# Kernel tuning notes

Hardware: AMD Instinct MI355X
Metric: run time of the kernel (lower is better)

The kernel has to match this reference:

```python
import jax, jax.numpy as jnp
import numpy as np

B, T, DIM = 1, 2048, 1024
NUM_HEADS, HEAD_DIM = 8, 128
ATTN_SCALE = 0.12


def _rms_norm(x):
    # F.rms_norm(x, x.size(-1)) with no weight; eps defaults to machine eps
    eps = jnp.asarray(jnp.finfo(x.dtype).eps, x.dtype)
    return x * jax.lax.rsqrt(jnp.mean(x * x, axis=-1, keepdims=True) + eps)


def _rotary_tables(seq_len, head_dim):
    # (1/1024) ** linspace(0,1,head_dim//4), then pad with head_dim//4 zeros
    freq = (1.0 / 1024.0) ** jnp.linspace(0.0, 1.0, head_dim // 4, dtype=jnp.float32)
    ang = jnp.concatenate([freq, jnp.zeros(head_dim // 4, jnp.float32)])  # [hd/2]
    theta = jnp.arange(seq_len, dtype=jnp.float32)[:, None] * ang[None, :]  # [T, hd/2]
    return jnp.cos(theta), jnp.sin(theta)


def _apply_rotary(x, cos, sin):
    # x: [B, T, H, hd]
    x1, x2 = jnp.split(x.astype(jnp.float32), 2, axis=-1)
    c = cos[None, :, None, :]
    s = sin[None, :, None, :]
    y1 = x1 * c + x2 * s
    y2 = -x1 * s + x2 * c
    return jnp.concatenate([y1, y2], axis=-1).astype(x.dtype)


def setup_inputs() -> dict:
    key = jax.random.key(0)
    ks = jax.random.split(key, 5)
    bound = (3.0 ** 0.5) * 0.5 * DIM ** (-0.5)
    x = jax.random.normal(ks[0], (B, T, DIM), jnp.float32)
    ve = jax.random.normal(ks[1], (B, T, NUM_HEADS * HEAD_DIM), jnp.float32)
    qkv_w = jax.random.uniform(ks[2], (3, NUM_HEADS * HEAD_DIM, DIM), jnp.float32, -bound, bound)
    lambdas = jnp.array([0.5, 0.5], jnp.float32)
    # original zero-inits c_proj; use small random weight so the output is nontrivial
    c_proj_w = jax.random.uniform(ks[3], (DIM, NUM_HEADS * HEAD_DIM), jnp.float32, -bound, bound)
    return {"x": x, "ve": ve, "qkv_w": qkv_w, "lambdas": lambdas, "c_proj_w": c_proj_w}


def reference(x, ve, qkv_w, lambdas, c_proj_w):
    Bx, Tx, D = x.shape
    H, hd = NUM_HEADS, HEAD_DIM
    # fused QKV projection: weight [3*H*hd, D]
    qkv = x @ qkv_w.reshape(3 * H * hd, D).T            # [B, T, 3*H*hd]
    qkv = qkv.reshape(Bx, Tx, 3 * H, hd)
    q, k, v = jnp.split(qkv, 3, axis=-2)                # each [B, T, H, hd]
    q, k = _rms_norm(q), _rms_norm(k)
    cos, sin = _rotary_tables(Tx, hd)
    q, k = _apply_rotary(q, cos, sin), _apply_rotary(k, cos, sin)
    v = lambdas[0] * v + lambdas[1] * ve.reshape(v.shape)
    att = jnp.einsum('bthd,bshd->bhts', q, k) * ATTN_SCALE
    causal = jnp.tril(jnp.ones((Tx, Tx), bool))
    att = jnp.where(causal[None, None], att, -jnp.inf)
    att = jax.nn.softmax(att, axis=-1)
    y = jnp.einsum('bhts,bshd->bthd', att, v).reshape(Bx, Tx, H * hd)
    return y @ c_proj_w.T
```

## Files before the change

### kernel.cpp

```cpp
#include <hip/hip_runtime.h>


typedef __attribute__((ext_vector_type(8))) short short8;
typedef __attribute__((ext_vector_type(4))) short short4b;
typedef __attribute__((ext_vector_type(4))) float fx4;
typedef __attribute__((ext_vector_type(8))) unsigned short ushort8;
typedef __attribute__((ext_vector_type(4))) unsigned short ushort4v;
typedef __attribute__((ext_vector_type(2))) unsigned short ushort2v;
typedef __attribute__((ext_vector_type(4))) float float4v;

#define T_SEQ 2048
#define NH 8
#define HD 128

__device__ __forceinline__ unsigned short f2bf(float f) {
  union { float f; unsigned u; } v; v.f = f;
  unsigned u = v.u;
  u += 0x7fffu + ((u >> 16) & 1u);
  return (unsigned short)(u >> 16);
}
__device__ __forceinline__ short bf_t(float f) {
  union { float f; unsigned u; } v; v.f = f;
  return (short)(v.u >> 16);
}
__device__ __forceinline__ float bf2f(unsigned short h) {
  union { unsigned u; float f; } v; v.u = ((unsigned)h) << 16;
  return v.f;
}

typedef __attribute__((address_space(1))) unsigned int glb_u32;
typedef __attribute__((address_space(3))) unsigned int lds_u32;
__device__ __forceinline__ void gl_lds16(const unsigned short* g, unsigned short* l) {
  __builtin_amdgcn_global_load_lds((const glb_u32*)g, (lds_u32*)l, 16, 0, 0);
}

__global__ __launch_bounds__(256) void cast3_kernel(
    const float* __restrict__ x, const float* __restrict__ w1,
    const float* __restrict__ w2, unsigned short* __restrict__ o) {
  long q = (long)blockIdx.x * 256 + threadIdx.x;
  const float* src;
  if (q < 524288)        src = x  + 4 * q;
  else if (q < 1310720)  src = w1 + 4 * (q - 524288);
  else                   src = w2 + 4 * (q - 1310720);
  float4v v = *(const float4v*)src;
  ushort4v r;
  r[0] = f2bf(v[0]); r[1] = f2bf(v[1]); r[2] = f2bf(v[2]); r[3] = f2bf(v[3]);
  *(ushort4v*)(o + 4 * q) = r;
}

template <bool OUT_BF16, int BM, int BN, int MINW>
__global__ __launch_bounds__(256, MINW) void gemm_bt4(
    const unsigned short* __restrict__ A, const unsigned short* __restrict__ B,
    void* __restrict__ Cp, int M, int N, int K) {
  constexpr int MT = BM / 32;
  constexpr int NT = BN / 32;
  constexpr int ASEG = BM / 8;
  constexpr int NLOAD = (BM + BN) / 32;
  __shared__ unsigned short a_sh[2][BM * 64];
  __shared__ unsigned short b_sh[2][BN * 64];
  const int tid = threadIdx.x;
  const int wave = tid >> 6, lane = tid & 63;
  const int ln = lane & 15, quad = lane >> 4;
  const int wm = wave & 1, wn = wave >> 1;
  const long arow0 = (long)blockIdx.y * BM;
  const long brow0 = (long)blockIdx.x * BN;

  const unsigned short* gsrc[NLOAD];
  unsigned short* ldst[NLOAD];
  int bstr[NLOAD];
  for (int i = 0; i < NLOAD; ++i) {
    int s = wave * NLOAD + i;
    int isB = s >= ASEG;
    int srel = isB ? s - ASEG : s;
    int li = srel * 64 + lane;
    int row = li >> 3, posc = li & 7;
    int c = posc ^ (row & 7);
    gsrc[i] = (isB ? B + brow0 * (long)K : A + arow0 * (long)K)
              + (long)row * K + c * 8;
    ldst[i] = (isB ? &b_sh[0][0] : &a_sh[0][0]) + srel * 512;
    bstr[i] = isB ? BN * 64 : BM * 64;
  }
  for (int i = 0; i < NLOAD; ++i) gl_lds16(gsrc[i], ldst[i]);

  fx4 acc[MT][NT] = {};
  int cur = 0;
  for (int k0 = 0; k0 < K; k0 += 64, cur ^= 1) {
    __syncthreads();
    if (k0 + 64 < K)
      for (int i = 0; i < NLOAD; ++i)
        gl_lds16(gsrc[i] + k0 + 64, ldst[i] + (cur ^ 1) * bstr[i]);
    const unsigned short* ash = &a_sh[cur][0];
    const unsigned short* bsh = &b_sh[cur][0];
    short8 af[2][MT], bfr[2][NT];
    for (int kq = 0; kq < 2; ++kq) {
      for (int mt = 0; mt < MT; ++mt) {
        int m = wm * (BM / 2) + mt * 16 + ln;
        int pos = (kq * 4 + quad) ^ (m & 7);
        af[kq][mt] = *(const short8*)&ash[m * 64 + pos * 8];
      }
      for (int nt = 0; nt < NT; ++nt) {
        int n = wn * (BN / 2) + nt * 16 + ln;
        int pos = (kq * 4 + quad) ^ (n & 7);
        bfr[kq][nt] = *(const short8*)&bsh[n * 64 + pos * 8];
      }
    }
    for (int kq = 0; kq < 2; ++kq)
      for (int mt = 0; mt < MT; ++mt)
        for (int nt = 0; nt < NT; ++nt)
          acc[mt][nt] = __builtin_amdgcn_mfma_f32_16x16x32_bf16(
              af[kq][mt], bfr[kq][nt], acc[mt][nt], 0, 0, 0);
  }
  for (int mt = 0; mt < MT; ++mt)
    for (int nt = 0; nt < NT; ++nt)
      for (int r = 0; r < 4; ++r) {
        long row = arow0 + wm * (BM / 2) + mt * 16 + quad * 4 + r;
        long col = brow0 + wn * (BN / 2) + nt * 16 + ln;
        float v = acc[mt][nt][r];
        if constexpr (OUT_BF16)
          ((unsigned short*)Cp)[row * N + col] = f2bf(v);
        else
          ((float*)Cp)[row * N + col] = v;
      }
}

__global__ __launch_bounds__(256) void prep_qkv(
    const unsigned short* __restrict__ qkv, const float* __restrict__ ve,
    const float* __restrict__ lambdas, unsigned short* __restrict__ qh,
    unsigned short* __restrict__ kh, unsigned short* __restrict__ vt) {
  __shared__ unsigned short lt[64 * 72];
  const int bx = blockIdx.x, h = blockIdx.y;
  const int tid = threadIdx.x;

  if (bx < 128) {
    const int r2 = tid >> 5, c = tid & 31;
    float ang[2];
    for (int u = 0; u < 2; ++u) {
      int dd = 2 * c + u;
      ang[u] = (dd < 32) ? exp2f(-10.0f * (float)dd / 31.0f) : 0.0f;
    }
    for (int rr = 0; rr < 2; ++rr) {
      int t = bx * 16 + rr * 8 + r2;
      float cv[2], sv[2];
      for (int u = 0; u < 2; ++u) {
        float th = (float)t * ang[u];
        sv[u] = __sinf(th); cv[u] = __cosf(th);
      }
      for (int which = 0; which < 2; ++which) {
        const unsigned short* src = qkv + (long)t * 3072 + which * 1024 + h * 128;
        ushort2v aa = *(const ushort2v*)(src + 2 * c);
        ushort2v bb = *(const ushort2v*)(src + 64 + 2 * c);
        float x1[2] = { bf2f(aa[0]), bf2f(aa[1]) };
        float x2[2] = { bf2f(bb[0]), bf2f(bb[1]) };
        float ss = x1[0]*x1[0] + x1[1]*x1[1] + x2[0]*x2[0] + x2[1]*x2[1];
        for (int off = 1; off < 32; off <<= 1) ss += __shfl_xor(ss, off);
        float rn = rsqrtf(ss * (1.0f / 128.0f) + 1.1920929e-7f);
        ushort2v o1, o2;
        for (int u = 0; u < 2; ++u) {
          float y1 = ( x1[u] * cv[u] + x2[u] * sv[u]) * rn;
          float y2 = (-x1[u] * sv[u] + x2[u] * cv[u]) * rn;
          o1[u] = f2bf(y1); o2[u] = f2bf(y2);
        }
        unsigned short* dst = (which ? kh : qh) + ((long)h * T_SEQ + t) * 128;
        *(ushort2v*)(dst + 2 * c) = o1;
        *(ushort2v*)(dst + 64 + 2 * c) = o2;
      }
    }
  } else {
    const int vb = bx - 128;
    const int jt = vb >> 1, dsub = vb & 1;
    const float l0 = lambdas[0], l1 = lambdas[1];
    const int r = tid >> 2, cb = (tid & 3) * 16;
    const unsigned short* vs = qkv + (long)(jt * 64 + r) * 3072 + 2048
                               + h * 128 + dsub * 64 + cb;
    const float* es = ve + (long)(jt * 64 + r) * 1024 + h * 128 + dsub * 64 + cb;
    ushort8 vv[2];
    for (int q = 0; q < 2; ++q) vv[q] = *(const ushort8*)(vs + 8 * q);
    float4v ee[4];
    for (int q = 0; q < 4; ++q) ee[q] = *(const float4v*)(es + 4 * q);
    for (int j = 0; j < 16; ++j) {
      float v = bf2f(vv[j >> 3][j & 7]) * l0 + ee[j >> 2][j & 3] * l1;
      lt[(cb + j) * 72 + r] = f2bf(v);
    }
    __syncthreads();
    const int dl = tid >> 2, quarter = tid & 3;
    const int d = dsub * 64 + dl;
    const int dt = d >> 4, lnn = d & 15;
    const int kh2 = quarter >> 1, half = quarter & 1;
    unsigned short* dstb = vt + (((long)h * 32 + jt) * 16 + kh2 * 8 + dt) * 512
                           + half * 4;
    const unsigned short* srcl = &lt[dl * 72];
    for (int g = 0; g < 4; ++g)
      *(ushort4v*)(dstb + (g * 16 + lnn) * 8) =
          *(const ushort4v*)(srcl + quarter * 16 + g * 4);
  }
}

#define ATT_C1 0.17312340490667562f
#define ATT_C2 23.083120654223415f

__global__ __launch_bounds__(256, 2) void attn_part(
    const unsigned short* __restrict__ qh, const unsigned short* __restrict__ kh,
    const unsigned short* __restrict__ vt, unsigned short* __restrict__ Yp,
    float* __restrict__ lp) {
  __shared__ unsigned short kbuf[2][8192];
  const int tid = threadIdx.x;
  const int wave = tid >> 6, lane = tid & 63;
  const int ln = lane & 15, quad = lane >> 4;
  const int qt = 15 - (int)blockIdx.x, h = blockIdx.y, ch = blockIdx.z;
  const int jmax = 2 * qt + 1;
  const int j0 = ch * 4;
  if (j0 > jmax) return;
  const int j1 = min(j0 + 3, jmax);

  int qg[2];
  short8 qf[2][4];
  for (int s = 0; s < 2; ++s) {
    qg[s] = qt * 128 + wave * 32 + s * 16 + ln;
    const unsigned short* qbase = qh + ((long)h * T_SEQ + qg[s]) * 128;
    for (int kc = 0; kc < 4; ++kc)
      qf[s][kc] = *(const short8*)(qbase + kc * 32 + quad * 8);
  }
  fx4 accy[2][8] = {};
  float l_loc[2] = {0.f, 0.f};

  const unsigned short* kg[4]; unsigned short* kl[4];
  for (int i = 0; i < 4; ++i) {
    int s = wave * 4 + i;
    int li = s * 64 + lane; int row = li >> 4, posc = li & 15;
    int c = posc ^ (row & 15);
    kg[i] = kh + ((long)h * T_SEQ + row) * 128 + c * 8;
    kl[i] = &kbuf[0][s * 512];
  }
  for (int i = 0; i < 4; ++i) gl_lds16(kg[i] + (long)j0 * 8192, kl[i]);

  const unsigned short* vlane = vt + ((long)h * 32) * 8192 + lane * 8;

  int cur = 0;
  for (int jt = j0; jt <= j1; ++jt, cur ^= 1) {
    __syncthreads();
    if (jt < j1)
      for (int i = 0; i < 4; ++i)
        gl_lds16(kg[i] + (long)(jt + 1) * 8192, kl[i] + (cur ^ 1) * 8192);
    const unsigned short* vb_ = vlane + (long)jt * 8192;
    short8 vf[16];
#pragma unroll
    for (int f = 0; f < 16; ++f) vf[f] = *(const short8*)(vb_ + f * 512);

    const unsigned short* kb_ = &kbuf[cur][0];
    fx4 s4[2][4];
    for (int kt = 0; kt < 4; ++kt) {
      s4[0][kt] = fx4{0.f, 0.f, 0.f, 0.f};
      s4[1][kt] = fx4{0.f, 0.f, 0.f, 0.f};
      for (int kc = 0; kc < 4; ++kc) {
        int pos = (kc * 4 + quad) ^ ln;
        short8 kf = *(const short8*)&kb_[(kt * 16 + ln) * 128 + pos * 8];
        s4[0][kt] = __builtin_amdgcn_mfma_f32_16x16x32_bf16(kf, qf[0][kc], s4[0][kt], 0, 0, 0);
        s4[1][kt] = __builtin_amdgcn_mfma_f32_16x16x32_bf16(kf, qf[1][kc], s4[1][kt], 0, 0, 0);
      }
    }
    short4b pb[2][4];
    for (int s = 0; s < 2; ++s)
      for (int kt = 0; kt < 4; ++kt) {
        int kvb = jt * 64 + kt * 16 + quad * 4;
        float p[4];
        for (int r = 0; r < 4; ++r)
          p[r] = exp2f(fmaf(s4[s][kt][r], ATT_C1, -ATT_C2));
        if (jt * 64 + kt * 16 + 15 > qt * 128 + wave * 32 + s * 16) {
          for (int r = 0; r < 4; ++r) if (kvb + r > qg[s]) p[r] = 0.f;
        }
        l_loc[s] += (p[0] + p[1]) + (p[2] + p[3]);
        pb[s][kt] = short4b{ bf_t(p[0]), bf_t(p[1]), bf_t(p[2]), bf_t(p[3]) };
      }
#pragma unroll
    for (int kh2 = 0; kh2 < 2; ++kh2) {
#pragma unroll
      for (int dt = 0; dt < 8; ++dt) {
        short8 va = vf[kh2 * 8 + dt];
        short4b va0 = { va[0], va[1], va[2], va[3] };
        short4b va1 = { va[4], va[5], va[6], va[7] };
        for (int s = 0; s < 2; ++s) {
          accy[s][dt] = __builtin_amdgcn_mfma_f32_16x16x16bf16_1k(
              va0, pb[s][kh2 * 2], accy[s][dt], 0, 0, 0);
          accy[s][dt] = __builtin_amdgcn_mfma_f32_16x16x16bf16_1k(
              va1, pb[s][kh2 * 2 + 1], accy[s][dt], 0, 0, 0);
        }
      }
    }
  }

  int cbase = qt + ((qt - 1) * (qt - 1)) / 4;
  const long pp = (long)(h * 72 + cbase + ch);
  for (int s = 0; s < 2; ++s) {
    float l = l_loc[s];
    l += __shfl_xor(l, 16);
    l += __shfl_xor(l, 32);
    int q = wave * 32 + s * 16 + ln;
    if (quad == 0) lp[pp * 128 + q] = l;
    unsigned short* yb = Yp + pp * 16384 + (long)q * 128;
    for (int dt = 0; dt < 8; ++dt) {
      ushort4v o;
      for (int r = 0; r < 4; ++r) o[r] = f2bf(accy[s][dt][r]);
      *(ushort4v*)(yb + dt * 16 + quad * 4) = o;
    }
  }
}

__global__ __launch_bounds__(256) void attn_combine(
    const unsigned short* __restrict__ Yp, const float* __restrict__ lp,
    unsigned short* __restrict__ y) {
  const int bx = blockIdx.x, h = blockIdx.y;
  const int tid = threadIdx.x;
  const int row = bx * 16 + (tid >> 4);
  const int cb  = (tid & 15) * 8;
  const int qt = row >> 7;
  const int r128 = row & 127;
  const int nc = (qt >> 1) + 1;
  const int cbase = qt + ((qt - 1) * (qt - 1)) / 4;
  float acc[8];
  for (int j = 0; j < 8; ++j) acc[j] = 0.f;
  float ltot = 0.f;
  for (int c = 0; c < nc; ++c) {
    long pp = (long)(h * 72 + cbase + c);
    const unsigned short* ys = Yp + pp * 16384 + (long)r128 * 128 + cb;
    ltot += lp[pp * 128 + r128];
    ushort8 v = *(const ushort8*)ys;
    for (int j = 0; j < 8; ++j) acc[j] += bf2f(v[j]);
  }
  float inv = 1.f / ltot;
  unsigned short* dst = y + (long)row * 1024 + h * 128 + cb;
  ushort8 o;
  for (int j = 0; j < 8; ++j) o[j] = f2bf(acc[j] * inv);
  *(ushort8*)dst = o;
}

extern "C" void kernel_launch(void* const* d_in, const int* in_sizes, int n_in,
                              void* d_out, int out_size, void* d_ws, size_t ws_size,
                              hipStream_t stream) {
  const float* x       = (const float*)d_in[0];
  const float* ve      = (const float*)d_in[1];
  const float* qkv_w   = (const float*)d_in[2];
  const float* lambdas = (const float*)d_in[3];
  const float* c_proj  = (const float*)d_in[4];
  char* ws = (char*)d_ws;
  unsigned short* qkv_bf = (unsigned short*)(ws);
  unsigned short* x_bf   = (unsigned short*)(ws + 12582912);
  unsigned short* wqkv   = (unsigned short*)(ws + 16777216);
  unsigned short* wproj  = (unsigned short*)(ws + 23068672);
  unsigned short* qhat   = (unsigned short*)(ws + 25165824);
  unsigned short* khat   = (unsigned short*)(ws + 29360128);
  unsigned short* vtb    = (unsigned short*)(ws + 33554432);
  unsigned short* ybf    = (unsigned short*)(ws + 37748736);
  unsigned short* Yp     = (unsigned short*)(ws);
  float*          lpart  = (float*)(ws + 18874368);
  float* out = (float*)d_out;

  cast3_kernel<<<6144, 256, 0, stream>>>(x, qkv_w, c_proj, x_bf);
  gemm_bt4<true, 64, 128, 3><<<dim3(24, 32), 256, 0, stream>>>(x_bf, wqkv, qkv_bf, 2048, 3072, 1024);
  prep_qkv<<<dim3(192, 8), 256, 0, stream>>>(qkv_bf, ve, lambdas, qhat, khat, vtb);
  attn_part<<<dim3(16, 8, 8), 256, 0, stream>>>(qhat, khat, vtb, Yp, lpart);
  attn_combine<<<dim3(128, 8), 256, 0, stream>>>(Yp, lpart, ybf);
  gemm_bt4<false, 32, 64, 4><<<dim3(16, 64), 256, 0, stream>>>(ybf, wproj, out, 2048, 1024, 1024);
}
```

Before: 169.2 us.

## Load K fragments directly from global memory instead of LDS double buffering

The attention kernel stops staging K tiles in a double-buffered LDS buffer and drops the per-iteration __syncthreads. Each wave now loads its K fragments straight from global memory into registers. V fragment loads are split into two halves so the second half is issued after the QK MFMAs, which lowers register pressure and overlaps load latency. The trade-off is that all four waves read the same K tile, so global/L2 traffic for K rises, and the global K reads are less coalesced than before.

```diff
diff --git a/kernel.cpp b/kernel.cpp
--- a/kernel.cpp
+++ b/kernel.cpp
@@ -202,7 +202,6 @@
     const unsigned short* __restrict__ qh, const unsigned short* __restrict__ kh,
     const unsigned short* __restrict__ vt, unsigned short* __restrict__ Yp,
     float* __restrict__ lp) {
-  __shared__ unsigned short kbuf[2][8192];
   const int tid = threadIdx.x;
   const int wave = tid >> 6, lane = tid & 63;
   const int ln = lane & 15, quad = lane >> 4;
@@ -223,41 +222,35 @@
   fx4 accy[2][8] = {};
   float l_loc[2] = {0.f, 0.f};
 
-  const unsigned short* kg[4]; unsigned short* kl[4];
-  for (int i = 0; i < 4; ++i) {
-    int s = wave * 4 + i;
-    int li = s * 64 + lane; int row = li >> 4, posc = li & 15;
-    int c = posc ^ (row & 15);
-    kg[i] = kh + ((long)h * T_SEQ + row) * 128 + c * 8;
-    kl[i] = &kbuf[0][s * 512];
-  }
-  for (int i = 0; i < 4; ++i) gl_lds16(kg[i] + (long)j0 * 8192, kl[i]);
-
+  const unsigned short* kbase = kh + (((long)h * T_SEQ + ln) << 7) + quad * 8;
   const unsigned short* vlane = vt + ((long)h * 32) * 8192 + lane * 8;
 
-  int cur = 0;
-  for (int jt = j0; jt <= j1; ++jt, cur ^= 1) {
-    __syncthreads();
-    if (jt < j1)
-      for (int i = 0; i < 4; ++i)
-        gl_lds16(kg[i] + (long)(jt + 1) * 8192, kl[i] + (cur ^ 1) * 8192);
+  for (int jt = j0; jt <= j1; ++jt) {
+    const unsigned short* kj = kbase + ((long)jt << 13);
     const unsigned short* vb_ = vlane + (long)jt * 8192;
-    short8 vf[16];
-#pragma unroll
-    for (int f = 0; f < 16; ++f) vf[f] = *(const short8*)(vb_ + f * 512);
-
-    const unsigned short* kb_ = &kbuf[cur][0];
+    short8 vfA[8];
+#pragma unroll
+    for (int f = 0; f < 8; ++f) vfA[f] = *(const short8*)(vb_ + f * 512);
+
     fx4 s4[2][4];
+#pragma unroll
     for (int kt = 0; kt < 4; ++kt) {
+      short8 kf[4];
+#pragma unroll
+      for (int kc = 0; kc < 4; ++kc)
+        kf[kc] = *(const short8*)(kj + (kt << 11) + kc * 32);
       s4[0][kt] = fx4{0.f, 0.f, 0.f, 0.f};
       s4[1][kt] = fx4{0.f, 0.f, 0.f, 0.f};
+#pragma unroll
       for (int kc = 0; kc < 4; ++kc) {
-        int pos = (kc * 4 + quad) ^ ln;
-        short8 kf = *(const short8*)&kb_[(kt * 16 + ln) * 128 + pos * 8];
-        s4[0][kt] = __builtin_amdgcn_mfma_f32_16x16x32_bf16(kf, qf[0][kc], s4[0][kt], 0, 0, 0);
-        s4[1][kt] = __builtin_amdgcn_mfma_f32_16x16x32_bf16(kf, qf[1][kc], s4[1][kt], 0, 0, 0);
-      }
-    }
+        s4[0][kt] = __builtin_amdgcn_mfma_f32_16x16x32_bf16(kf[kc], qf[0][kc], s4[0][kt], 0, 0, 0);
+        s4[1][kt] = __builtin_amdgcn_mfma_f32_16x16x32_bf16(kf[kc], qf[1][kc], s4[1][kt], 0, 0, 0);
+      }
+    }
+    short8 vfB[8];
+#pragma unroll
+    for (int f = 0; f < 8; ++f) vfB[f] = *(const short8*)(vb_ + (8 + f) * 512);
+
     short4b pb[2][4];
     for (int s = 0; s < 2; ++s)
       for (int kt = 0; kt < 4; ++kt) {
@@ -272,18 +265,27 @@
         pb[s][kt] = short4b{ bf_t(p[0]), bf_t(p[1]), bf_t(p[2]), bf_t(p[3]) };
       }
 #pragma unroll
-    for (int kh2 = 0; kh2 < 2; ++kh2) {
-#pragma unroll
-      for (int dt = 0; dt < 8; ++dt) {
-        short8 va = vf[kh2 * 8 + dt];
-        short4b va0 = { va[0], va[1], va[2], va[3] };
-        short4b va1 = { va[4], va[5], va[6], va[7] };
-        for (int s = 0; s < 2; ++s) {
-          accy[s][dt] = __builtin_amdgcn_mfma_f32_16x16x16bf16_1k(
-              va0, pb[s][kh2 * 2], accy[s][dt], 0, 0, 0);
-          accy[s][dt] = __builtin_amdgcn_mfma_f32_16x16x16bf16_1k(
-              va1, pb[s][kh2 * 2 + 1], accy[s][dt], 0, 0, 0);
-        }
+    for (int dt = 0; dt < 8; ++dt) {
+      short8 va = vfA[dt];
+      short4b va0 = { va[0], va[1], va[2], va[3] };
+      short4b va1 = { va[4], va[5], va[6], va[7] };
+      for (int s = 0; s < 2; ++s) {
+        accy[s][dt] = __builtin_amdgcn_mfma_f32_16x16x16bf16_1k(
+            va0, pb[s][0], accy[s][dt], 0, 0, 0);
+        accy[s][dt] = __builtin_amdgcn_mfma_f32_16x16x16bf16_1k(
+            va1, pb[s][1], accy[s][dt], 0, 0, 0);
+      }
+    }
+#pragma unroll
+    for (int dt = 0; dt < 8; ++dt) {
+      short8 va = vfB[dt];
+      short4b va0 = { va[0], va[1], va[2], va[3] };
+      short4b va1 = { va[4], va[5], va[6], va[7] };
+      for (int s = 0; s < 2; ++s) {
+        accy[s][dt] = __builtin_amdgcn_mfma_f32_16x16x16bf16_1k(
+            va0, pb[s][2], accy[s][dt], 0, 0, 0);
+        accy[s][dt] = __builtin_amdgcn_mfma_f32_16x16x16bf16_1k(
+            va1, pb[s][3], accy[s][dt], 0, 0, 0);
       }
     }
   }
```

Result: slower. 182.9 us (+8.1%).

## Fuse all stages into one cooperative persistent kernel with grid syncs

Applied to the files above, without the earlier changes.

Replaces six separate kernel launches with a single cooperative persistent kernel of 512 blocks. The blocks loop over virtual tiles for each stage and separate the stages with grid.sync(). The QKV GEMM tile changes from 64x128 to 64x64, and the kernel falls back to the old multi-launch path if the cooperative launch fails. The aim is to remove launch gaps and tail effects between stages. In exchange it adds grid-wide barrier cost, caps occupancy at 2 blocks per CU with a shared 64KB LDS buffer, and loses per-kernel launch-bound tuning.

```diff
diff --git a/kernel.cpp b/kernel.cpp
--- a/kernel.cpp
+++ b/kernel.cpp
@@ -1,4 +1,6 @@
 #include <hip/hip_runtime.h>
+#include <hip/hip_cooperative_groups.h>
+namespace cg = cooperative_groups;
 
 
 typedef __attribute__((ext_vector_type(8))) short short8;
@@ -12,6 +14,7 @@
 #define T_SEQ 2048
 #define NH 8
 #define HD 128
+#define NBLK 512
 
 __device__ __forceinline__ unsigned short f2bf(float f) {
   union { float f; unsigned u; } v; v.f = f;
@@ -34,36 +37,26 @@
   __builtin_amdgcn_global_load_lds((const glb_u32*)g, (lds_u32*)l, 16, 0, 0);
 }
 
-__global__ __launch_bounds__(256) void cast3_kernel(
-    const float* __restrict__ x, const float* __restrict__ w1,
-    const float* __restrict__ w2, unsigned short* __restrict__ o) {
-  long q = (long)blockIdx.x * 256 + threadIdx.x;
-  const float* src;
-  if (q < 524288)        src = x  + 4 * q;
-  else if (q < 1310720)  src = w1 + 4 * (q - 524288);
-  else                   src = w2 + 4 * (q - 1310720);
-  float4v v = *(const float4v*)src;
-  ushort4v r;
-  r[0] = f2bf(v[0]); r[1] = f2bf(v[1]); r[2] = f2bf(v[2]); r[3] = f2bf(v[3]);
-  *(ushort4v*)(o + 4 * q) = r;
-}
-
-template <bool OUT_BF16, int BM, int BN, int MINW>
-__global__ __launch_bounds__(256, MINW) void gemm_bt4(
-    const unsigned short* __restrict__ A, const unsigned short* __restrict__ B,
-    void* __restrict__ Cp, int M, int N, int K) {
+#define ATT_C1 0.17312340490667562f
+#define ATT_C2 23.083120654223415f
+
+template <bool OUT_BF16, int BM, int BN>
+__device__ void gemm_tile(const unsigned short* __restrict__ A,
+                          const unsigned short* __restrict__ B,
+                          void* __restrict__ Cp, int M, int N, int K,
+                          int bxi, int byi, unsigned short* smem) {
   constexpr int MT = BM / 32;
   constexpr int NT = BN / 32;
   constexpr int ASEG = BM / 8;
   constexpr int NLOAD = (BM + BN) / 32;
-  __shared__ unsigned short a_sh[2][BM * 64];
-  __shared__ unsigned short b_sh[2][BN * 64];
+  unsigned short* a_sh = smem;
+  unsigned short* b_sh = smem + 2 * BM * 64;
   const int tid = threadIdx.x;
   const int wave = tid >> 6, lane = tid & 63;
   const int ln = lane & 15, quad = lane >> 4;
   const int wm = wave & 1, wn = wave >> 1;
-  const long arow0 = (long)blockIdx.y * BM;
-  const long brow0 = (long)blockIdx.x * BN;
+  const long arow0 = (long)byi * BM;
+  const long brow0 = (long)bxi * BN;
 
   const unsigned short* gsrc[NLOAD];
   unsigned short* ldst[NLOAD];
@@ -77,7 +70,7 @@
     int c = posc ^ (row & 7);
     gsrc[i] = (isB ? B + brow0 * (long)K : A + arow0 * (long)K)
               + (long)row * K + c * 8;
-    ldst[i] = (isB ? &b_sh[0][0] : &a_sh[0][0]) + srel * 512;
+    ldst[i] = (isB ? b_sh : a_sh) + srel * 512;
     bstr[i] = isB ? BN * 64 : BM * 64;
   }
   for (int i = 0; i < NLOAD; ++i) gl_lds16(gsrc[i], ldst[i]);
@@ -89,8 +82,8 @@
     if (k0 + 64 < K)
       for (int i = 0; i < NLOAD; ++i)
         gl_lds16(gsrc[i] + k0 + 64, ldst[i] + (cur ^ 1) * bstr[i]);
-    const unsigned short* ash = &a_sh[cur][0];
-    const unsigned short* bsh = &b_sh[cur][0];
+    const unsigned short* ash = a_sh + cur * BM * 64;
+    const unsigned short* bsh = b_sh + cur * BN * 64;
     short8 af[2][MT], bfr[2][NT];
     for (int kq = 0; kq < 2; ++kq) {
       for (int mt = 0; mt < MT; ++mt) {
@@ -110,6 +103,7 @@
           acc[mt][nt] = __builtin_amdgcn_mfma_f32_16x16x32_bf16(
               af[kq][mt], bfr[kq][nt], acc[mt][nt], 0, 0, 0);
   }
+  __syncthreads();
   for (int mt = 0; mt < MT; ++mt)
     for (int nt = 0; nt < NT; ++nt)
       for (int r = 0; r < 4; ++r) {
@@ -123,14 +117,14 @@
       }
 }
 
-__global__ __launch_bounds__(256) void prep_qkv(
-    const unsigned short* __restrict__ qkv, const float* __restrict__ ve,
-    const float* __restrict__ lambdas, unsigned short* __restrict__ qh,
-    unsigned short* __restrict__ kh, unsigned short* __restrict__ vt) {
-  __shared__ unsigned short lt[64 * 72];
-  const int bx = blockIdx.x, h = blockIdx.y;
+__device__ void prep_body(const unsigned short* __restrict__ qkv,
+                          const float* __restrict__ ve,
+                          const float* __restrict__ lambdas,
+                          unsigned short* __restrict__ qh,
+                          unsigned short* __restrict__ kh,
+                          unsigned short* __restrict__ vt,
+                          int bx, int h, unsigned short* smem) {
   const int tid = threadIdx.x;
-
   if (bx < 128) {
     const int r2 = tid >> 5, c = tid & 31;
     float ang[2];
@@ -166,8 +160,9 @@
       }
     }
   } else {
-    const int vb = bx - 128;
-    const int jt = vb >> 1, dsub = vb & 1;
+    unsigned short* lt = smem;
+    const int vb2 = bx - 128;
+    const int jt = vb2 >> 1, dsub = vb2 & 1;
     const float l0 = lambdas[0], l1 = lambdas[1];
     const int r = tid >> 2, cb = (tid & 3) * 16;
     const unsigned short* vs = qkv + (long)(jt * 64 + r) * 3072 + 2048
@@ -195,21 +190,18 @@
   }
 }
 
-#define ATT_C1 0.17312340490667562f
-#define ATT_C2 23.083120654223415f
-
-__global__ __launch_bounds__(256, 2) void attn_part(
-    const unsigned short* __restrict__ qh, const unsigned short* __restrict__ kh,
-    const unsigned short* __restrict__ vt, unsigned short* __restrict__ Yp,
-    float* __restrict__ lp) {
-  __shared__ unsigned short kbuf[2][8192];
+__device__ void attn_body(const unsigned short* __restrict__ qh,
+                          const unsigned short* __restrict__ kh,
+                          const unsigned short* __restrict__ vt,
+                          unsigned short* __restrict__ Yp,
+                          float* __restrict__ lp,
+                          int qt, int h, int ch, unsigned short* smem) {
+  unsigned short* kbuf = smem;
   const int tid = threadIdx.x;
   const int wave = tid >> 6, lane = tid & 63;
   const int ln = lane & 15, quad = lane >> 4;
-  const int qt = 15 - (int)blockIdx.x, h = blockIdx.y, ch = blockIdx.z;
   const int jmax = 2 * qt + 1;
   const int j0 = ch * 4;
-  if (j0 > jmax) return;
   const int j1 = min(j0 + 3, jmax);
 
   int qg[2];
@@ -229,7 +221,7 @@
     int li = s * 64 + lane; int row = li >> 4, posc = li & 15;
     int c = posc ^ (row & 15);
     kg[i] = kh + ((long)h * T_SEQ + row) * 128 + c * 8;
-    kl[i] = &kbuf[0][s * 512];
+    kl[i] = &kbuf[s * 512];
   }
   for (int i = 0; i < 4; ++i) gl_lds16(kg[i] + (long)j0 * 8192, kl[i]);
 
@@ -246,7 +238,7 @@
 #pragma unroll
     for (int f = 0; f < 16; ++f) vf[f] = *(const short8*)(vb_ + f * 512);
 
-    const unsigned short* kb_ = &kbuf[cur][0];
+    const unsigned short* kb_ = &kbuf[cur * 8192];
     fx4 s4[2][4];
     for (int kt = 0; kt < 4; ++kt) {
       s4[0][kt] = fx4{0.f, 0.f, 0.f, 0.f};
@@ -305,10 +297,9 @@
   }
 }
 
-__global__ __launch_bounds__(256) void attn_combine(
-    const unsigned short* __restrict__ Yp, const float* __restrict__ lp,
-    unsigned short* __restrict__ y) {
-  const int bx = blockIdx.x, h = blockIdx.y;
+__device__ void combine_body(const unsigned short* __restrict__ Yp,
+                             const float* __restrict__ lp,
+                             unsigned short* __restrict__ y, int bx, int h) {
   const int tid = threadIdx.x;
   const int row = bx * 16 + (tid >> 4);
   const int cb  = (tid & 15) * 8;
@@ -331,6 +322,115 @@
   ushort8 o;
   for (int j = 0; j < 8; ++j) o[j] = f2bf(acc[j] * inv);
   *(ushort8*)dst = o;
+}
+
+__global__ __launch_bounds__(256, 2) void mega(
+    const float* __restrict__ x, const float* __restrict__ ve,
+    const float* __restrict__ lambdas,
+    const float* __restrict__ qkv_w, const float* __restrict__ c_proj,
+    unsigned short* __restrict__ x_bf, unsigned short* __restrict__ wqkv,
+    unsigned short* __restrict__ wproj,
+    unsigned short* __restrict__ qkv_bf,
+    unsigned short* __restrict__ qh, unsigned short* __restrict__ kh,
+    unsigned short* __restrict__ vt,
+    unsigned short* __restrict__ Yp, float* __restrict__ lp,
+    unsigned short* __restrict__ ybf, float* __restrict__ out) {
+  cg::grid_group grid = cg::this_grid();
+  __shared__ unsigned short smem[32768];
+  const int bid = blockIdx.x;
+  const int tid = threadIdx.x;
+
+  for (int u = bid; u < 6144; u += NBLK) {
+    long q = (long)u * 256 + tid;
+    const float* src;
+    if (q < 524288)        src = x      + 4 * q;
+    else if (q < 1310720)  src = qkv_w  + 4 * (q - 524288);
+    else                   src = c_proj + 4 * (q - 1310720);
+    float4v v = *(const float4v*)src;
+    ushort4v r;
+    r[0] = f2bf(v[0]); r[1] = f2bf(v[1]); r[2] = f2bf(v[2]); r[3] = f2bf(v[3]);
+    *(ushort4v*)(x_bf + 4 * q) = r;
+  }
+  grid.sync();
+
+  for (int vb = bid; vb < 1536; vb += NBLK) {
+    __syncthreads();
+    gemm_tile<true, 64, 64>(x_bf, wqkv, qkv_bf, 2048, 3072, 1024,
+                            vb % 48, vb / 48, smem);
+  }
+  grid.sync();
+
+  for (int vb = bid; vb < 1536; vb += NBLK) {
+    __syncthreads();
+    prep_body(qkv_bf, ve, lambdas, qh, kh, vt, vb % 192, vb / 192, smem);
+  }
+  grid.sync();
+
+  for (int vb = bid; vb < 1024; vb += NBLK) {
+    __syncthreads();
+    const int qt = 15 - (vb & 15);
+    const int h = (vb >> 4) & 7;
+    const int ch = vb >> 7;
+    if (ch * 4 <= 2 * qt + 1)
+      attn_body(qh, kh, vt, Yp, lp, qt, h, ch, smem);
+  }
+  grid.sync();
+
+  for (int vb = bid; vb < 1024; vb += NBLK)
+    combine_body(Yp, lp, ybf, vb & 127, vb >> 7);
+  grid.sync();
+
+  for (int vb = bid; vb < 1024; vb += NBLK) {
+    __syncthreads();
+    gemm_tile<false, 32, 64>(ybf, wproj, out, 2048, 1024, 1024,
+                             vb % 16, vb / 16, smem);
+  }
+}
+
+__global__ __launch_bounds__(256) void cast3_kernel(
+    const float* __restrict__ x, const float* __restrict__ w1,
+    const float* __restrict__ w2, unsigned short* __restrict__ o) {
+  long q = (long)blockIdx.x * 256 + threadIdx.x;
+  const float* src;
+  if (q < 524288)        src = x  + 4 * q;
+  else if (q < 1310720)  src = w1 + 4 * (q - 524288);
+  else                   src = w2 + 4 * (q - 1310720);
+  float4v v = *(const float4v*)src;
+  ushort4v r;
+  r[0] = f2bf(v[0]); r[1] = f2bf(v[1]); r[2] = f2bf(v[2]); r[3] = f2bf(v[3]);
+  *(ushort4v*)(o + 4 * q) = r;
+}
+
+template <bool OUT_BF16, int BM, int BN, int MINW>
+__global__ __launch_bounds__(256, MINW) void gemm_bt4(
+    const unsigned short* __restrict__ A, const unsigned short* __restrict__ B,
+    void* __restrict__ Cp, int M, int N, int K) {
+  __shared__ unsigned short smem[2 * BM * 64 + 2 * BN * 64];
+  gemm_tile<OUT_BF16, BM, BN>(A, B, Cp, M, N, K, blockIdx.x, blockIdx.y, smem);
+}
+
+__global__ __launch_bounds__(256) void prep_qkv(
+    const unsigned short* __restrict__ qkv, const float* __restrict__ ve,
+    const float* __restrict__ lambdas, unsigned short* __restrict__ qh,
+    unsigned short* __restrict__ kh, unsigned short* __restrict__ vt) {
+  __shared__ unsigned short lt[64 * 72];
+  prep_body(qkv, ve, lambdas, qh, kh, vt, blockIdx.x, blockIdx.y, lt);
+}
+
+__global__ __launch_bounds__(256, 2) void attn_part(
+    const unsigned short* __restrict__ qh, const unsigned short* __restrict__ kh,
+    const unsigned short* __restrict__ vt, unsigned short* __restrict__ Yp,
+    float* __restrict__ lp) {
+  __shared__ unsigned short kbuf[2 * 8192];
+  const int qt = 15 - (int)blockIdx.x, h = blockIdx.y, ch = blockIdx.z;
+  if (ch * 4 > 2 * qt + 1) return;
+  attn_body(qh, kh, vt, Yp, lp, qt, h, ch, kbuf);
+}
+
+__global__ __launch_bounds__(256) void attn_combine(
+    const unsigned short* __restrict__ Yp, const float* __restrict__ lp,
+    unsigned short* __restrict__ y) {
+  combine_body(Yp, lp, y, blockIdx.x, blockIdx.y);
 }
 
 extern "C" void kernel_launch(void* const* d_in, const int* in_sizes, int n_in,
@@ -354,10 +454,21 @@
   float*          lpart  = (float*)(ws + 18874368);
   float* out = (float*)d_out;
 
-  cast3_kernel<<<6144, 256, 0, stream>>>(x, qkv_w, c_proj, x_bf);
-  gemm_bt4<true, 64, 128, 3><<<dim3(24, 32), 256, 0, stream>>>(x_bf, wqkv, qkv_bf, 2048, 3072, 1024);
-  prep_qkv<<<dim3(192, 8), 256, 0, stream>>>(qkv_bf, ve, lambdas, qhat, khat, vtb);
-  attn_part<<<dim3(16, 8, 8), 256, 0, stream>>>(qhat, khat, vtb, Yp, lpart);
-  attn_combine<<<dim3(128, 8), 256, 0, stream>>>(Yp, lpart, ybf);
-  gemm_bt4<false, 32, 64, 4><<<dim3(16, 64), 256, 0, stream>>>(ybf, wproj, out, 2048, 1024, 1024);
-}
+  void* args[] = {
+    (void*)&x, (void*)&ve, (void*)&lambdas,
+    (void*)&qkv_w, (void*)&c_proj,
+    (void*)&x_bf, (void*)&wqkv, (void*)&wproj,
+    (void*)&qkv_bf, (void*)&qhat, (void*)&khat, (void*)&vtb,
+    (void*)&Yp, (void*)&lpart, (void*)&ybf, (void*)&out
+  };
+  hipError_t err = hipLaunchCooperativeKernel(
+      (void*)mega, dim3(NBLK), dim3(256), args, 0, stream);
+  if (err != hipSuccess) {
+    cast3_kernel<<<6144, 256, 0, stream>>>(x, qkv_w, c_proj, x_bf);
+    gemm_bt4<true, 64, 128, 3><<<dim3(24, 32), 256, 0, stream>>>(x_bf, wqkv, qkv_bf, 2048, 3072, 1024);
+    prep_qkv<<<dim3(192, 8), 256, 0, stream>>>(qkv_bf, ve, lambdas, qhat, khat, vtb);
+    attn_part<<<dim3(16, 8, 8), 256, 0, stream>>>(qhat, khat, vtb, Yp, lpart);
+    attn_combine<<<dim3(128, 8), 256, 0, stream>>>(Yp, lpart, ybf);
+    gemm_bt4<false, 32, 64, 4><<<dim3(16, 64), 256, 0, stream>>>(ybf, wproj, out, 2048, 1024, 1024);
+  }
+}
```

Measured after the change: 512.9 us. 3.03x slower.
